# Kernel optimization log

Hardware: AMD Instinct MI355X
Metric: run time of the kernel (lower is better)

Reference implementation:

```python
import jax, jax.numpy as jnp
import numpy as np
from jax import lax

DIM = 1024
HEADS = 16
KERNEL = 7
STRIDE = 4
EPS = 1e-5


def setup_inputs() -> dict:
    key = jax.random.key(0)
    ks = jax.random.split(key, 4)
    B, N = 2, 4096
    w_scale = 0.02
    return {
        "x": jax.random.normal(ks[0], (B, N, DIM), dtype=jnp.float32),
        "ln_w": jnp.ones((DIM,), jnp.float32),
        "ln_b": jnp.zeros((DIM,), jnp.float32),
        "Wk": jax.random.normal(ks[1], (DIM, DIM, KERNEL), dtype=jnp.float32) * w_scale,
        "Wv": jax.random.normal(ks[2], (DIM, DIM, KERNEL), dtype=jnp.float32) * w_scale,
        "Wq": jax.random.normal(ks[3], (DIM, DIM, KERNEL), dtype=jnp.float32) * w_scale,
    }


def _conv1d(x_bnd, w):
    # x: (B, N, D) -> conv over sequence dim with 'same' padding; w: (out_ch, in_ch, K)
    x_cn = jnp.transpose(x_bnd, (0, 2, 1))  # (B, D, N)
    pad = KERNEL // 2
    y = lax.conv_general_dilated(
        x_cn, w, window_strides=(1,), padding=[(pad, pad)],
        dimension_numbers=("NCH", "OIH", "NCH"))
    return jnp.transpose(y, (0, 2, 1))  # (B, N, D)


def reference(x, ln_w, ln_b, Wk, Wv, Wq):
    B, N, D = x.shape
    hd = D // HEADS
    # LayerNorm (biased variance, as in torch)
    mu = jnp.mean(x, axis=-1, keepdims=True)
    var = jnp.mean(jnp.square(x - mu), axis=-1, keepdims=True)
    x_n = (x - mu) / jnp.sqrt(var + EPS) * ln_w + ln_b

    K = _conv1d(x_n, Wk)                 # (B, N, D)
    V = _conv1d(x_n, Wv)                 # (B, N, D)
    Q = _conv1d(x_n, Wq)[:, ::STRIDE]    # (B, M, D) windowed queries
    M = Q.shape[1]

    Qh = Q.reshape(B, M, HEADS, hd).transpose(0, 2, 1, 3)  # (B, H, M, hd)
    Kh = K.reshape(B, N, HEADS, hd).transpose(0, 2, 1, 3)  # (B, H, N, hd)
    Vh = V.reshape(B, N, HEADS, hd).transpose(0, 2, 1, 3)  # (B, H, N, hd)

    scale = jnp.sqrt(jnp.asarray(hd, x.dtype))
    scores = jnp.einsum("bhmd,bhnd->bhmn", Qh, Kh) / scale  # (B, H, M, N)
    attn = jax.nn.softmax(scores, axis=-1)
    out = jnp.einsum("bhmn,bhnd->bhmd", attn, Vh)           # (B, H, M, hd)
    out = out.transpose(0, 2, 1, 3).reshape(B, M, D)
    return out + Q
```

## Files before the change

### kernel.cpp

```cpp
#include <hip/hip_runtime.h>

typedef __attribute__((ext_vector_type(4))) float f32x4;
typedef __attribute__((ext_vector_type(8))) short short8;
typedef __attribute__((ext_vector_type(4))) unsigned short u16x4;

#define AS1 __attribute__((address_space(1)))
#define AS3 __attribute__((address_space(3)))

__device__ __forceinline__ unsigned short f2bf(float f) {
  unsigned u = __float_as_uint(f);
  return (unsigned short)((u + 0x7FFFu + ((u >> 16) & 1u)) >> 16);
}
__device__ __forceinline__ unsigned short f2bf_fast(float f) {
  return (unsigned short)((__float_as_uint(f) + 0x8000u) >> 16);
}

__global__ __launch_bounds__(256) void ln_kernel(
    const float* __restrict__ x, const float* __restrict__ lw,
    const float* __restrict__ lb, unsigned short* __restrict__ xpad) {
  __shared__ float red[8];
  int row = blockIdx.x;
  int b = row >> 12, n = row & 4095;
  const float* xr = x + (size_t)row * 1024;
  int c = threadIdx.x * 4;
  f32x4 v = *(const f32x4*)(xr + c);
  float s = v[0] + v[1] + v[2] + v[3];
  float sq = v[0]*v[0] + v[1]*v[1] + v[2]*v[2] + v[3]*v[3];
#pragma unroll
  for (int off = 32; off; off >>= 1) {
    s  += __shfl_xor(s, off, 64);
    sq += __shfl_xor(sq, off, 64);
  }
  int w = threadIdx.x >> 6;
  if ((threadIdx.x & 63) == 0) { red[w*2] = s; red[w*2+1] = sq; }
  __syncthreads();
  float S  = red[0]+red[2]+red[4]+red[6];
  float SQ = red[1]+red[3]+red[5]+red[7];
  float mean = S * (1.0f/1024.0f);
  float var  = SQ * (1.0f/1024.0f) - mean*mean;
  float rstd = rsqrtf(var + 1e-5f);
  f32x4 wv = *(const f32x4*)(lw + c);
  f32x4 bv = *(const f32x4*)(lb + c);
  u16x4 o;
#pragma unroll
  for (int r = 0; r < 4; ++r) o[r] = f2bf((v[r]-mean)*rstd*wv[r] + bv[r]);
  *(u16x4*)(xpad + (((size_t)(b*4102 + n + 3)) << 10) + c) = o;
}

__global__ __launch_bounds__(256) void repack_kernel(
    const float* __restrict__ Wk, const float* __restrict__ Wv,
    const float* __restrict__ Wq, unsigned short* __restrict__ Wt) {
  __shared__ unsigned short t[7168];
  const float* W = (blockIdx.y == 0) ? Wk : (blockIdx.y == 1) ? Wv : Wq;
  int o = blockIdx.x;
  const float* row = W + (size_t)o * 7168;
  unsigned short* orow = Wt + ((size_t)(blockIdx.y * 1024 + o)) * 7168;
#pragma unroll
  for (int p = 0; p < 7; ++p) {
    int idx = p*1024 + threadIdx.x*4;
    f32x4 v = *(const f32x4*)(row + idx);
#pragma unroll
    for (int e = 0; e < 4; ++e) {
      unsigned j = idx + e;
      unsigned i = (j * 149797u) >> 20;
      unsigned k = j - i*7;
      t[k*1024 + i] = f2bf(v[e]);
    }
  }
  __syncthreads();
#pragma unroll
  for (int p = 0; p < 7; ++p) {
    int idx = p*1024 + threadIdx.x*4;
    *(u16x4*)(orow + idx) = *(const u16x4*)(t + idx);
  }
}

__global__ __launch_bounds__(512, 2) void conv256(
    const unsigned short* __restrict__ Apad,
    const unsigned short* __restrict__ Wt,
    unsigned short* __restrict__ Ksg, unsigned short* __restrict__ Vsg,
    float* __restrict__ Qp) {
  __shared__ unsigned short As[2][2][8192];
  __shared__ unsigned short Bs[2][2][8192];

  const int tid = threadIdx.x;
  const int w = tid >> 6, l = tid & 63;
  const int wm = w >> 2, wn = w & 3;
  const int l15 = l & 15, lh4 = l >> 4, l7 = l & 7;
  const int chA = ((l7 & 4) | (lh4 ^ (l7 & 3))) << 3;
  const int wOff = w << 9;
  const int bid = blockIdx.x;
  const int xcd = bid & 7, j = bid >> 3;
  const int ct = j & 7, rt = (xcd << 2) | (j >> 3);

  unsigned aOff[2][2], bOff[2][2];
#pragma unroll
  for (int i = 0; i < 2; ++i) {
    const int idx = i * 512 + tid;
    const int r = idx >> 3;
    const int clog8 = (((idx & 7) ^ (r & 7)) << 3);
#pragma unroll
    for (int hh = 0; hh < 2; ++hh) {
      const int rg = (rt << 8) + (hh << 7) + r;
      aOff[hh][i] = ((unsigned)((rg >> 12) * 4102 + (rg & 4095)) << 10) + clog8;
      const int cg = (ct << 8) + (hh << 7) + r;
      bOff[hh][i] = (unsigned)cg * 7168u + clog8;
    }
  }

  unsigned aRd[4], bRd[2];
#pragma unroll
  for (int fm = 0; fm < 4; ++fm)
    aRd[fm] = (unsigned)(((wm << 6) + (fm << 4) + l15) << 6) + chA;
#pragma unroll
  for (int fn = 0; fn < 2; ++fn)
    bRd[fn] = (unsigned)(((wn << 5) + (fn << 4) + l15) << 6) + chA;

  f32x4 acc[2][2][4][2] = {};
  short8 af[4][2], bfr[2][2];

#define STGA(BUF, HALF, T) do { \
    __builtin_amdgcn_global_load_lds((const AS1 void*)(Apad + aOff[HALF][0] + ((unsigned)(T) << 6)), (AS3 void*)&As[BUF][HALF][wOff], 16, 0, 0); \
    __builtin_amdgcn_global_load_lds((const AS1 void*)(Apad + aOff[HALF][1] + ((unsigned)(T) << 6)), (AS3 void*)&As[BUF][HALF][4096 + wOff], 16, 0, 0); \
  } while (0)
#define STGB(BUF, HALF, T) do { \
    __builtin_amdgcn_global_load_lds((const AS1 void*)(Wt + bOff[HALF][0] + ((unsigned)(T) << 6)), (AS3 void*)&Bs[BUF][HALF][wOff], 16, 0, 0); \
    __builtin_amdgcn_global_load_lds((const AS1 void*)(Wt + bOff[HALF][1] + ((unsigned)(T) << 6)), (AS3 void*)&Bs[BUF][HALF][4096 + wOff], 16, 0, 0); \
  } while (0)
#define LDA(BUF, MQ) do { \
    _Pragma("unroll") for (int fm = 0; fm < 4; ++fm) { \
      af[fm][0] = *(const short8*)&As[BUF][MQ][aRd[fm]]; \
      af[fm][1] = *(const short8*)&As[BUF][MQ][aRd[fm] ^ 32u]; } \
  } while (0)
#define LDB(BUF, NQ) do { \
    _Pragma("unroll") for (int fn = 0; fn < 2; ++fn) { \
      bfr[fn][0] = *(const short8*)&Bs[BUF][NQ][bRd[fn]]; \
      bfr[fn][1] = *(const short8*)&Bs[BUF][NQ][bRd[fn] ^ 32u]; } \
  } while (0)
#define MM(MQ, NQ) do { \
    _Pragma("unroll") for (int ks = 0; ks < 2; ++ks) \
    _Pragma("unroll") for (int fm = 0; fm < 4; ++fm) \
    _Pragma("unroll") for (int fn = 0; fn < 2; ++fn) \
      acc[MQ][NQ][fm][fn] = __builtin_amdgcn_mfma_f32_16x16x32_bf16(af[fm][ks], bfr[fn][ks], acc[MQ][NQ][fm][fn], 0, 0, 0); \
  } while (0)
#define BAR __builtin_amdgcn_s_barrier()
#define LGKM0 asm volatile("s_waitcnt lgkmcnt(0)" ::: "memory")
#define VM6 asm volatile("s_waitcnt vmcnt(6)" ::: "memory")
#define VM0 asm volatile("s_waitcnt vmcnt(0)" ::: "memory")
#define P1 __builtin_amdgcn_s_setprio(1)
#define P0 __builtin_amdgcn_s_setprio(0)

#define RUN_GEMM(NIT) do { \
    STGA(0, 0, 0); STGB(0, 0, 0); STGA(0, 1, 0); STGB(0, 1, 0); \
    STGA(1, 0, 1); STGB(1, 1, 1); STGA(1, 1, 1); \
    VM6; BAR; \
    for (int I = 0; I < (NIT) - 1; ++I) { \
      const int t0 = I * 2; \
      LDA(0, 0); LDB(0, 0); STGB(1, 0, t0 + 1); \
      BAR; LGKM0; P1; MM(0, 0); P0; BAR; \
      LDB(0, 1);            STGA(0, 0, t0 + 2); \
      BAR; LGKM0; P1; MM(0, 1); P0; BAR; \
      LDA(0, 1);            STGB(0, 1, t0 + 2); \
      BAR; LGKM0; P1; MM(1, 1); P0; BAR; \
      LDB(0, 0);            STGA(0, 1, t0 + 2); \
      BAR; LGKM0; P1; MM(1, 0); P0; VM6; BAR; \
      LDA(1, 0); LDB(1, 0); STGB(0, 0, t0 + 2); \
      BAR; LGKM0; P1; MM(0, 0); P0; BAR; \
      LDB(1, 1);            STGA(1, 0, t0 + 3); \
      BAR; LGKM0; P1; MM(0, 1); P0; BAR; \
      LDA(1, 1);            STGB(1, 1, t0 + 3); \
      BAR; LGKM0; P1; MM(1, 1); P0; BAR; \
      LDB(1, 0);            STGA(1, 1, t0 + 3); \
      BAR; LGKM0; P1; MM(1, 0); P0; VM6; BAR; \
    } \
    { \
      LDA(0, 0); LDB(0, 0); STGB(1, 0, ((NIT) - 1) * 2 + 1); \
      BAR; LGKM0; P1; MM(0, 0); P0; BAR; \
      LDB(0, 1); BAR; LGKM0; P1; MM(0, 1); P0; BAR; \
      LDA(0, 1); BAR; LGKM0; P1; MM(1, 1); P0; BAR; \
      LDB(0, 0); BAR; LGKM0; P1; MM(1, 0); P0; VM0; BAR; \
      LDA(1, 0); LDB(1, 0); BAR; LGKM0; P1; MM(0, 0); P0; BAR; \
      LDB(1, 1); BAR; LGKM0; P1; MM(0, 1); P0; BAR; \
      LDA(1, 1); BAR; LGKM0; P1; MM(1, 1); P0; BAR; \
      LDB(1, 0); BAR; LGKM0; P1; MM(1, 0); P0; BAR; \
    } \
  } while (0)

  RUN_GEMM(56);

  if (ct < 4) {
#pragma unroll
    for (int mq = 0; mq < 2; ++mq)
#pragma unroll
      for (int nq = 0; nq < 2; ++nq) {
        const int h = (ct << 2) + (nq << 1) + (wn >> 1);
        const int kd = wn & 1;
#pragma unroll
        for (int fm = 0; fm < 4; ++fm) {
          const int rbase = (rt << 8) + (mq << 7) + (wm << 6) + (fm << 4) + (lh4 << 2);
          const int b = rbase >> 12, n0 = rbase & 4095;
          const size_t base = ((((size_t)((b * 16 + h) * 2 + kd)) << 12) + n0) << 5;
#pragma unroll
          for (int fn = 0; fn < 2; ++fn) {
            const int d32 = (fn << 4) + l15;
#pragma unroll
            for (int rr = 0; rr < 4; ++rr)
              Ksg[base + ((size_t)rr << 5) + d32] = f2bf(acc[mq][nq][fm][fn][rr]);
          }
        }
      }
  } else {
#pragma unroll
    for (int mq = 0; mq < 2; ++mq)
#pragma unroll
      for (int nq = 0; nq < 2; ++nq) {
        const int h = ((ct - 4) << 2) + (nq << 1) + (wn >> 1);
        const int dhi = (wn & 1) << 5;
#pragma unroll
        for (int fm = 0; fm < 4; ++fm) {
          const int rbase = (rt << 8) + (mq << 7) + (wm << 6) + (fm << 4) + (lh4 << 2);
          const int b = rbase >> 12, n = rbase & 4095;
#pragma unroll
          for (int fn = 0; fn < 2; ++fn) {
            const int d = dhi + (fn << 4) + l15;
            const size_t rowbase =
                ((((((size_t)(b * 16 + h)) << 7) + (n >> 5)) << 6) + d) * 32 + (n & 31);
            u16x4 pv;
#pragma unroll
            for (int rr = 0; rr < 4; ++rr) pv[rr] = f2bf(acc[mq][nq][fm][fn][rr]);
            *(u16x4*)(Vsg + rowbase) = pv;
          }
        }
      }
  }

  const int qct = j & 3, qrt = j >> 2, kc = xcd;
  const unsigned kbase = (unsigned)kc * 896u;
#pragma unroll
  for (int i = 0; i < 2; ++i) {
    const int idx = i * 512 + tid;
    const int r = idx >> 3;
    const int clog8 = (((idx & 7) ^ (r & 7)) << 3);
#pragma unroll
    for (int hh = 0; hh < 2; ++hh) {
      const int rg = (qrt << 8) + (hh << 7) + r;
      aOff[hh][i] = ((unsigned)((rg >> 10) * 4102 + ((rg & 1023) << 2)) << 10) + clog8 + kbase;
      const int cg = 2048 + (qct << 8) + (hh << 7) + r;
      bOff[hh][i] = (unsigned)cg * 7168u + clog8 + kbase;
    }
  }
#pragma unroll
  for (int mq = 0; mq < 2; ++mq)
#pragma unroll
    for (int nq = 0; nq < 2; ++nq)
#pragma unroll
      for (int fm = 0; fm < 4; ++fm)
#pragma unroll
        for (int fn = 0; fn < 2; ++fn)
          acc[mq][nq][fm][fn] = (f32x4){0.f, 0.f, 0.f, 0.f};

  RUN_GEMM(7);

  float* Qc = Qp + ((size_t)kc << 21);
#pragma unroll
  for (int mq = 0; mq < 2; ++mq)
#pragma unroll
    for (int nq = 0; nq < 2; ++nq)
#pragma unroll
      for (int fm = 0; fm < 4; ++fm) {
        const int rq = (qrt << 8) + (mq << 7) + (wm << 6) + (fm << 4) + (lh4 << 2);
#pragma unroll
        for (int fn = 0; fn < 2; ++fn) {
          const int cq = (qct << 8) + (nq << 7) + (wn << 5) + (fn << 4) + l15;
#pragma unroll
          for (int rr = 0; rr < 4; ++rr)
            Qc[(((size_t)(rq + rr)) << 10) + cq] = acc[mq][nq][fm][fn][rr];
        }
      }
#undef STGA
#undef STGB
#undef LDA
#undef LDB
#undef MM
#undef BAR
#undef LGKM0
#undef VM6
#undef VM0
#undef P1
#undef P0
#undef RUN_GEMM
}

__global__ __launch_bounds__(256) void qfinal(
    const float* __restrict__ Qp, float* __restrict__ Qf,
    unsigned short* __restrict__ Qsg) {
  const int rq = blockIdx.x;
  const int b = rq >> 10, m = rq & 1023;
  const int c = threadIdx.x << 2;
  f32x4 v = {0.f, 0.f, 0.f, 0.f};
#pragma unroll
  for (int kc = 0; kc < 8; ++kc) {
    f32x4 p = *(const f32x4*)(Qp + ((size_t)kc << 21) + ((size_t)rq << 10) + c);
    v[0] += p[0]; v[1] += p[1]; v[2] += p[2]; v[3] += p[3];
  }
  *(f32x4*)(Qf + ((size_t)rq << 10) + c) = v;
  const int h = c >> 6, kd = (c >> 5) & 1, d32 = c & 31;
  u16x4 o;
#pragma unroll
  for (int e = 0; e < 4; ++e) o[e] = f2bf(v[e]);
  *(u16x4*)(Qsg + ((((size_t)((b * 16 + h) * 2 + kd)) << 10) + m) * 32 + d32) = o;
}

__global__ __launch_bounds__(512) void attn_kernel(
    const unsigned short* __restrict__ Ksg, const unsigned short* __restrict__ Vsg,
    const unsigned short* __restrict__ Qsg, const float* __restrict__ Qf,
    float* __restrict__ out) {
  __shared__ unsigned short Ks[2][8192];
  __shared__ unsigned short Vs[2][8192];
  __shared__ unsigned short Qs[8192];
  __shared__ unsigned short Ps[2][17408];
  const int tid = threadIdx.x, w = tid >> 6, l = tid & 63;
  const int g = blockIdx.x;
  const int bh = (g & 7) + (((g >> 3) & 3) << 3);
  const int qt = g >> 5;
  const int b = bh >> 4, h = bh & 15;
  const int m0 = qt << 7;
  const int quad = l >> 4, lc = l & 15, l3 = l & 3;
  const float C = 0.18033688011112042f;
  const int lsw = (l & 60) | ((l ^ (l >> 2)) & 3);
  const int ch = (quad ^ l3) << 3;

  const unsigned short* KgT = Ksg + ((size_t)bh << 18);
  const unsigned short* VgT = Vsg + ((size_t)bh << 18);
  const unsigned short* QgT = Qsg + ((size_t)bh << 16);

#pragma unroll
  for (int p = 0; p < 2; ++p) {
    int t = (w << 1) + p;
    int kd = t >> 3, ml = (t & 7) << 4;
    __builtin_amdgcn_global_load_lds(
        (const AS1 void*)(QgT + ((size_t)((kd << 10) + m0 + ml) << 5) + lsw*8),
        (AS3 void*)(Qs + (t << 9)), 16, 0, 0);
  }

#define STAGE_KV(BUF, N0) do { \
    _Pragma("unroll") for (int p = 0; p < 2; ++p) { \
      int t = (w << 1) + p; \
      __builtin_amdgcn_global_load_lds( \
          (const AS1 void*)(KgT + ((size_t)(((t >> 3) << 12) + (N0) + ((t & 7) << 4)) << 5) + lsw*8), \
          (AS3 void*)(Ks[BUF] + (t << 9)), 16, 0, 0); \
      __builtin_amdgcn_global_load_lds( \
          (const AS1 void*)(VgT + ((size_t)(((((N0) >> 5) + (t >> 2)) << 6) + ((t & 3) << 4)) << 5) + lsw*8), \
          (AS3 void*)(Vs[BUF] + (t << 9)), 16, 0, 0); \
    } \
  } while (0)

  float l_run = 0.f;
  f32x4 oacc[4] = {};
  short8 vfrag[4][4];

  STAGE_KV(0, 0);
  asm volatile("s_waitcnt vmcnt(0)" ::: "memory");
  __builtin_amdgcn_s_barrier();

  for (int it = 0; it < 32; ++it) {
    const int cur = it & 1;
    const unsigned short* Kc = Ks[cur];
    const unsigned short* Vc = Vs[cur];
    if (it < 31) STAGE_KV(cur ^ 1, (it + 1) << 7);

    if (it > 0) {
      unsigned short* Pp = Ps[cur ^ 1] + w*2176;
#pragma unroll
      for (int kn = 0; kn < 4; ++kn) {
        short8 bp = *(const short8*)(Pp + lc*136 + (kn<<5) + (quad<<3));
#pragma unroll
        for (int dt = 0; dt < 4; ++dt)
          oacc[dt] = __builtin_amdgcn_mfma_f32_16x16x32_bf16(vfrag[kn][dt], bp, oacc[dt], 0, 0, 0);
      }
    }

    short8 ak[8][2];
#pragma unroll
    for (int k = 0; k < 2; ++k)
#pragma unroll
      for (int ni = 0; ni < 8; ++ni)
        ak[ni][k] = *(const short8*)(Kc + (k << 12) + ((ni<<4) + lc)*32 + ch);

    f32x4 sv[8] = {};
#pragma unroll
    for (int k = 0; k < 2; ++k) {
      short8 bq = *(const short8*)(Qs + (k << 12) + ((w<<4) + lc)*32 + ch);
#pragma unroll
      for (int ni = 0; ni < 8; ++ni)
        sv[ni] = __builtin_amdgcn_mfma_f32_16x16x32_bf16(ak[ni][k], bq, sv[ni], 0, 0, 0);
    }

#pragma unroll
    for (int kn = 0; kn < 4; ++kn)
#pragma unroll
      for (int dt = 0; dt < 4; ++dt)
        vfrag[kn][dt] = *(const short8*)(Vc + (kn << 11) + ((dt<<4) + lc)*32 + ch);

    unsigned short* Pw = Ps[cur] + w*2176;
    float su = 0.f;
#pragma unroll
    for (int ni = 0; ni < 8; ++ni) {
      u16x4 pv;
#pragma unroll
      for (int rr = 0; rr < 4; ++rr) {
        float pp = __builtin_amdgcn_exp2f(sv[ni][rr] * C);
        su += pp;
        pv[rr] = f2bf_fast(pp);
      }
      *(u16x4*)(Pw + lc*136 + (ni<<4) + (quad<<2)) = pv;
    }
    su += __shfl_xor(su, 16, 64);
    su += __shfl_xor(su, 32, 64);
    l_run += su;

    asm volatile("s_waitcnt vmcnt(0)" ::: "memory");
    __builtin_amdgcn_s_barrier();
  }

  {
    unsigned short* Pp = Ps[1] + w*2176;
#pragma unroll
    for (int kn = 0; kn < 4; ++kn) {
      short8 bp = *(const short8*)(Pp + lc*136 + (kn<<5) + (quad<<3));
#pragma unroll
      for (int dt = 0; dt < 4; ++dt)
        oacc[dt] = __builtin_amdgcn_mfma_f32_16x16x32_bf16(vfrag[kn][dt], bp, oacc[dt], 0, 0, 0);
    }
  }
#undef STAGE_KV

  float invl = 1.0f / l_run;
  int m = m0 + (w<<4) + lc;
#pragma unroll
  for (int dt = 0; dt < 4; ++dt) {
    int d = (dt<<4) + (quad<<2);
    size_t off = (((size_t)(b << 10) + m) << 10) + (h << 6) + d;
    f32x4 qv = *(const f32x4*)(Qf + off);
    f32x4 ov;
#pragma unroll
    for (int rr = 0; rr < 4; ++rr) ov[rr] = oacc[dt][rr]*invl + qv[rr];
    *(f32x4*)(out + off) = ov;
  }
}

extern "C" void kernel_launch(void* const* d_in, const int* in_sizes, int n_in,
                              void* d_out, int out_size, void* d_ws, size_t ws_size,
                              hipStream_t stream) {
  const float* x  = (const float*)d_in[0];
  const float* lw = (const float*)d_in[1];
  const float* lb = (const float*)d_in[2];
  const float* Wk = (const float*)d_in[3];
  const float* Wv = (const float*)d_in[4];
  const float* Wq = (const float*)d_in[5];
  float* out = (float*)d_out;

  char* ws = (char*)d_ws;
  size_t off = 0;
  unsigned short* xpad = (unsigned short*)(ws + off); off += (size_t)2*4102*1024*2;
  unsigned short* Wt   = (unsigned short*)(ws + off); off += (size_t)3072*7168*2;
  unsigned short* Ksg  = (unsigned short*)(ws + off); off += (size_t)32*2*4096*32*2;
  unsigned short* Vsg  = (unsigned short*)(ws + off); off += (size_t)32*128*64*32*2;
  unsigned short* Qsg  = (unsigned short*)(ws + off); off += (size_t)32*2*1024*32*2;
  float*          Qf   = (float*)(ws + off);          off += (size_t)2048*1024*4;
  float*          Qp   = (float*)(ws + off);          off += (size_t)8*2048*1024*4;

  for (int b = 0; b < 2; ++b) {
    hipMemsetAsync(xpad + (size_t)b*4102*1024, 0, 3*1024*2, stream);
    hipMemsetAsync(xpad + ((size_t)b*4102 + 4099)*1024, 0, 3*1024*2, stream);
  }
  ln_kernel<<<dim3(8192), dim3(256), 0, stream>>>(x, lw, lb, xpad);
  repack_kernel<<<dim3(1024, 3), dim3(256), 0, stream>>>(Wk, Wv, Wq, Wt);
  conv256<<<dim3(256), dim3(512), 0, stream>>>(xpad, Wt, Ksg, Vsg, Qp);
  qfinal<<<dim3(2048), dim3(256), 0, stream>>>(Qp, Qf, Qsg);
  attn_kernel<<<dim3(256), dim3(512), 0, stream>>>(Ksg, Vsg, Qsg, Qf, out);
}
```

Baseline: 477.8 us.

## Load V fragments directly from global into registers, skipping LDS staging

V tiles are no longer staged into shared memory through global_load_lds. Each lane now reads its V MFMA fragments straight from global memory with a swizzled column offset, which frees the Vs LDS buffers. Q fragments are hoisted out of the loop, and the row-sum cross-lane shuffle reduction moves from every iteration to the end. The direct V loads put global latency on the loop's critical path and rely on the s_waitcnt before the barrier. They also change the access pattern, with possible uncoalesced reads.

```diff
diff --git a/kernel.cpp b/kernel.cpp
--- a/kernel.cpp
+++ b/kernel.cpp
@@ -316,7 +316,6 @@
     const unsigned short* __restrict__ Qsg, const float* __restrict__ Qf,
     float* __restrict__ out) {
   __shared__ unsigned short Ks[2][8192];
-  __shared__ unsigned short Vs[2][8192];
   __shared__ unsigned short Qs[8192];
   __shared__ unsigned short Ps[2][17408];
   const int tid = threadIdx.x, w = tid >> 6, l = tid & 63;
@@ -329,6 +328,7 @@
   const float C = 0.18033688011112042f;
   const int lsw = (l & 60) | ((l ^ (l >> 2)) & 3);
   const int ch = (quad ^ l3) << 3;
+  const int vch = (quad ^ l3 ^ (lc & 3)) << 3;
 
   const unsigned short* KgT = Ksg + ((size_t)bh << 18);
   const unsigned short* VgT = Vsg + ((size_t)bh << 18);
@@ -343,31 +343,32 @@
         (AS3 void*)(Qs + (t << 9)), 16, 0, 0);
   }
 
-#define STAGE_KV(BUF, N0) do { \
+#define STAGE_K(BUF, N0) do { \
     _Pragma("unroll") for (int p = 0; p < 2; ++p) { \
       int t = (w << 1) + p; \
       __builtin_amdgcn_global_load_lds( \
           (const AS1 void*)(KgT + ((size_t)(((t >> 3) << 12) + (N0) + ((t & 7) << 4)) << 5) + lsw*8), \
           (AS3 void*)(Ks[BUF] + (t << 9)), 16, 0, 0); \
-      __builtin_amdgcn_global_load_lds( \
-          (const AS1 void*)(VgT + ((size_t)(((((N0) >> 5) + (t >> 2)) << 6) + ((t & 3) << 4)) << 5) + lsw*8), \
-          (AS3 void*)(Vs[BUF] + (t << 9)), 16, 0, 0); \
     } \
   } while (0)
 
-  float l_run = 0.f;
+  float su_acc = 0.f;
   f32x4 oacc[4] = {};
   short8 vfrag[4][4];
 
-  STAGE_KV(0, 0);
+  STAGE_K(0, 0);
   asm volatile("s_waitcnt vmcnt(0)" ::: "memory");
   __builtin_amdgcn_s_barrier();
+
+  short8 bq[2];
+#pragma unroll
+  for (int k = 0; k < 2; ++k)
+    bq[k] = *(const short8*)(Qs + (k << 12) + ((w<<4) + lc)*32 + ch);
 
   for (int it = 0; it < 32; ++it) {
     const int cur = it & 1;
     const unsigned short* Kc = Ks[cur];
-    const unsigned short* Vc = Vs[cur];
-    if (it < 31) STAGE_KV(cur ^ 1, (it + 1) << 7);
+    if (it < 31) STAGE_K(cur ^ 1, (it + 1) << 7);
 
     if (it > 0) {
       unsigned short* Pp = Ps[cur ^ 1] + w*2176;
@@ -380,6 +381,15 @@
       }
     }
 
+    {
+      const unsigned short* Vb = VgT + ((size_t)it << 13);
+#pragma unroll
+      for (int kn = 0; kn < 4; ++kn)
+#pragma unroll
+        for (int dt = 0; dt < 4; ++dt)
+          vfrag[kn][dt] = *(const short8*)(Vb + (kn << 11) + ((dt<<4) + lc)*32 + vch);
+    }
+
     short8 ak[8][2];
 #pragma unroll
     for (int k = 0; k < 2; ++k)
@@ -389,35 +399,23 @@
 
     f32x4 sv[8] = {};
 #pragma unroll
-    for (int k = 0; k < 2; ++k) {
-      short8 bq = *(const short8*)(Qs + (k << 12) + ((w<<4) + lc)*32 + ch);
+    for (int k = 0; k < 2; ++k)
 #pragma unroll
       for (int ni = 0; ni < 8; ++ni)
-        sv[ni] = __builtin_amdgcn_mfma_f32_16x16x32_bf16(ak[ni][k], bq, sv[ni], 0, 0, 0);
-    }
-
-#pragma unroll
-    for (int kn = 0; kn < 4; ++kn)
-#pragma unroll
-      for (int dt = 0; dt < 4; ++dt)
-        vfrag[kn][dt] = *(const short8*)(Vc + (kn << 11) + ((dt<<4) + lc)*32 + ch);
+        sv[ni] = __builtin_amdgcn_mfma_f32_16x16x32_bf16(ak[ni][k], bq[k], sv[ni], 0, 0, 0);
 
     unsigned short* Pw = Ps[cur] + w*2176;
-    float su = 0.f;
 #pragma unroll
     for (int ni = 0; ni < 8; ++ni) {
       u16x4 pv;
 #pragma unroll
       for (int rr = 0; rr < 4; ++rr) {
         float pp = __builtin_amdgcn_exp2f(sv[ni][rr] * C);
-        su += pp;
+        su_acc += pp;
         pv[rr] = f2bf_fast(pp);
       }
       *(u16x4*)(Pw + lc*136 + (ni<<4) + (quad<<2)) = pv;
     }
-    su += __shfl_xor(su, 16, 64);
-    su += __shfl_xor(su, 32, 64);
-    l_run += su;
 
     asm volatile("s_waitcnt vmcnt(0)" ::: "memory");
     __builtin_amdgcn_s_barrier();
@@ -433,9 +431,11 @@
         oacc[dt] = __builtin_amdgcn_mfma_f32_16x16x32_bf16(vfrag[kn][dt], bp, oacc[dt], 0, 0, 0);
     }
   }
-#undef STAGE_KV
-
-  float invl = 1.0f / l_run;
+#undef STAGE_K
+
+  su_acc += __shfl_xor(su_acc, 16, 64);
+  su_acc += __shfl_xor(su_acc, 32, 64);
+  float invl = 1.0f / su_acc;
   int m = m0 + (w<<4) + lc;
 #pragma unroll
   for (int dt = 0; dt < 4; ++dt) {
```

Result: slower. 497.1 us (+4.0%).
